# Performance work log

Measured on AMD Instinct MI355X. Metric: run time of the kernel, lower is better.

Reference implementation:

```python
import jax, jax.numpy as jnp
import numpy as np

N, L, DS, DP, H, A, Q, V = 1, 512, 384, 256, 12, 16, 4, 8
SHID = H * (DP + A + 3 * V + V)  # 3648
WC = float(np.sqrt(2.0 / (9.0 * Q)))
WL = float(np.sqrt(1.0 / 3.0))
EPS = 1e-5


def quat2rot(q):
    # q: (..., 3) partial quaternion (w fixed to 1, then normalized) -> (..., 3, 3)
    ones = jnp.ones(q.shape[:-1] + (1,), q.dtype)
    qf = jnp.concatenate([ones, q], axis=-1)
    qf = qf / jnp.linalg.norm(qf, axis=-1, keepdims=True)
    w, x, y, z = qf[..., 0], qf[..., 1], qf[..., 2], qf[..., 3]
    r0 = jnp.stack([1 - 2 * (y * y + z * z), 2 * (x * y - w * z), 2 * (x * z + w * y)], -1)
    r1 = jnp.stack([2 * (x * y + w * z), 1 - 2 * (x * x + z * z), 2 * (y * z - w * x)], -1)
    r2 = jnp.stack([2 * (x * z - w * y), 2 * (y * z + w * x), 1 - 2 * (x * x + y * y)], -1)
    return jnp.stack([r0, r1, r2], axis=-2)


def layer_norm(x, g, b):
    m = x.mean(-1, keepdims=True)
    v = ((x - m) ** 2).mean(-1, keepdims=True)
    return (x - m) / jnp.sqrt(v + EPS) * g + b


def setup_inputs() -> dict:
    key = jax.random.key(0)
    ks = jax.random.split(key, 24)
    w = lambda k, shape, s=0.02: (jax.random.normal(k, shape, jnp.float32) * s)
    return {
        'sfea': jax.random.normal(ks[0], (N, L, DS), jnp.float32),
        'pfea': jax.random.normal(ks[1], (N, L, L, DP), jnp.float32),
        'quat': jax.random.normal(ks[2], (N, L, 3), jnp.float32) * 0.1,
        'trsl': jax.random.normal(ks[3], (N, L, 3), jnp.float32),
        'Wq': w(ks[4], (DS, H * A)), 'Wk': w(ks[5], (DS, H * A)), 'Wv': w(ks[6], (DS, H * A)),
        'Wqp': w(ks[7], (DS, H * Q * 3)), 'Wkp': w(ks[8], (DS, H * Q * 3)), 'Wvp': w(ks[9], (DS, H * V * 3)),
        'Wb': w(ks[10], (DP, H)),
        'scale': jnp.ones((H,), jnp.float32),
        'Ws': w(ks[11], (SHID, DS)), 'bs': jnp.zeros((DS,), jnp.float32),
        'W1': w(ks[12], (DS, DS)), 'b1': jnp.zeros((DS,), jnp.float32),
        'W2': w(ks[13], (DS, DS)), 'b2': jnp.zeros((DS,), jnp.float32),
        'W3': w(ks[14], (DS, DS)), 'b3': jnp.zeros((DS,), jnp.float32),
        'g1': jnp.ones((DS,), jnp.float32), 'be1': jnp.zeros((DS,), jnp.float32),
        'g2': jnp.ones((DS,), jnp.float32), 'be2': jnp.zeros((DS,), jnp.float32),
    }


def reference(sfea, pfea, quat, trsl, Wq, Wk, Wv, Wqp, Wkp, Wvp, Wb, scale, Ws, bs,
              W1, b1, W2, b2, W3, b3, g1, be1, g2, be2):
    n, l = sfea.shape[0], sfea.shape[1]
    # projections
    q = (sfea @ Wq).reshape(n, l, H, A)
    k = (sfea @ Wk).reshape(n, l, H, A)
    v = (sfea @ Wv).reshape(n, l, H, A)
    qp = (sfea @ Wqp).reshape(n, l, H, Q, 3)
    kp = (sfea @ Wkp).reshape(n, l, H, Q, 3)
    vp = (sfea @ Wvp).reshape(n, l, H, V, 3)
    b = jnp.einsum('nijp,ph->nijh', pfea, Wb)
    # local frames
    rot = quat2rot(quat)  # (n, l, 3, 3)
    t = trsl[:, :, None, None, :]
    qp_g = jnp.einsum('nlij,nlhqj->nlhqi', rot, qp) + t
    kp_g = jnp.einsum('nlij,nlhqj->nlhqi', rot, kp) + t
    vp_g = jnp.einsum('nlij,nlhvj->nlhvi', rot, vp) + t
    # attention logits
    qk = jnp.einsum('nihd,njhd->nijh', q, k) / np.sqrt(A)
    diff = qp_g[:, :, None] - kp_g[:, None]  # (n, i, j, h, q, 3)
    d2 = jnp.sum(diff * diff, axis=(-1, -2))  # (n, i, j, h)
    qkp = (WC * jax.nn.softplus(scale) / 2.0) * d2
    a = jax.nn.softmax(WL * (qk + b - qkp), axis=2)  # (n, i, j, h)
    # weighted sums (einsum avoids huge broadcast intermediates)
    op = jnp.einsum('nijh,nijp->nihp', a, pfea)
    ov = jnp.einsum('nijh,njhd->nihd', a, v)
    ovp_g = jnp.einsum('nijh,njhvc->nihvc', a, vp_g)
    # map back into local frame: R^T (x - t)
    ovp = jnp.einsum('nlji,nlhvj->nlhvi', rot, ovp_g - t)
    ovp_norm = jnp.sqrt(jnp.sum(ovp * ovp, axis=-1))  # (n, l, h, v)
    shid = jnp.concatenate([op, ov, ovp.reshape(n, l, H, V * 3), ovp_norm], axis=-1)
    shid = shid.reshape(n, l, SHID)
    # output projection + residual, post-LN, MLP, post-LN (v1 path, p_drop=0)
    s = sfea + shid @ Ws + bs
    s = layer_norm(s, g1, be1)
    h = jax.nn.relu(s @ W1 + b1)
    h = jax.nn.relu(h @ W2 + b2)
    s = s + (h @ W3 + b3)
    s = layer_norm(s, g2, be2)
    return s
```

## Files before the change

kernel.cpp:

```cpp
#include <hip/hip_runtime.h>
#include <cstddef>

typedef __attribute__((ext_vector_type(8))) short short8;
typedef __attribute__((ext_vector_type(4))) float f32x4;

#define WC_CONST 0.2357022603955158f
#define WL_CONST 0.5773502691896258f

__device__ __forceinline__ unsigned short rne_bf16(float f) {
  unsigned int u = __float_as_uint(f);
  u += 0x7fffu + ((u >> 16) & 1u);
  return (unsigned short)(u >> 16);
}

__global__ __launch_bounds__(256) void concat_w_kernel(
    const float* __restrict__ Wq, const float* __restrict__ Wk, const float* __restrict__ Wv,
    const float* __restrict__ Wqp, const float* __restrict__ Wkp, const float* __restrict__ Wvp,
    float* __restrict__ Wcat) {
  int idx = blockIdx.x * 256 + threadIdx.x;
  if (idx >= 384 * 1152) return;
  int k = idx / 1152, c = idx % 1152;
  float v;
  if (c < 192)       v = Wq [k*192 + c];
  else if (c < 384)  v = Wk [k*192 + (c-192)];
  else if (c < 576)  v = Wv [k*192 + (c-384)];
  else if (c < 720)  v = Wqp[k*144 + (c-576)];
  else if (c < 864)  v = Wkp[k*144 + (c-720)];
  else               v = Wvp[k*288 + (c-864)];
  Wcat[idx] = v;
}

__global__ __launch_bounds__(256) void gemm64_kernel(
    const float* __restrict__ Amat, const float* __restrict__ Bmat, float* __restrict__ Cp,
    int M, int N, int K, int ksl) {
  __shared__ float As[16][68];
  __shared__ float Bs[16][68];
  int t = threadIdx.x;
  int bn = blockIdx.x, bm = blockIdx.y, bz = blockIdx.z;
  int k0 = bz * ksl;
  int tr = t >> 4, tc = t & 15;
  int lm = t >> 2, lk4 = (t & 3) << 2;
  int lkb = t >> 4, lnq = (t & 15) << 2;
  const float* Ab = Amat + (size_t)(bm*64 + lm) * K;
  const float* Bb = Bmat + bn*64 + lnq;
  float acc[4][4];
  #pragma unroll
  for (int a2 = 0; a2 < 4; a2++)
    #pragma unroll
    for (int b2 = 0; b2 < 4; b2++) acc[a2][b2] = 0.f;

  for (int k = k0; k < k0 + ksl; k += 16) {
    float4 av = *(const float4*)(Ab + k + lk4);
    float4 bv = *(const float4*)(Bb + (size_t)(k + lkb) * N);
    As[lk4+0][lm] = av.x; As[lk4+1][lm] = av.y; As[lk4+2][lm] = av.z; As[lk4+3][lm] = av.w;
    *(float4*)&Bs[lkb][lnq] = bv;
    __syncthreads();
    #pragma unroll
    for (int kk = 0; kk < 16; kk++) {
      float4 a4 = *(const float4*)&As[kk][tr << 2];
      float4 b4 = *(const float4*)&Bs[kk][tc << 2];
      float ar[4] = {a4.x, a4.y, a4.z, a4.w};
      float br[4] = {b4.x, b4.y, b4.z, b4.w};
      #pragma unroll
      for (int a2 = 0; a2 < 4; a2++)
        #pragma unroll
        for (int b2 = 0; b2 < 4; b2++) acc[a2][b2] += ar[a2] * br[b2];
    }
    __syncthreads();
  }
  float* Cb = Cp + (size_t)bz * M * N + (size_t)(bm*64 + (tr << 2)) * N + bn*64 + (tc << 2);
  #pragma unroll
  for (int r = 0; r < 4; r++) {
    float4 o = {acc[r][0], acc[r][1], acc[r][2], acc[r][3]};
    *(float4*)(Cb + (size_t)r * N) = o;
  }
}

__global__ __launch_bounds__(256) void reduce_kernel(
    const float* __restrict__ Cp, float* __restrict__ out, const float* __restrict__ bias,
    int relu, int MN, int N, int sk) {
  int idx = blockIdx.x * 256 + threadIdx.x;
  if (idx >= MN) return;
  float s = 0.f;
  for (int z = 0; z < sk; z++) s += Cp[(size_t)z * MN + idx];
  if (bias) s += bias[idx % N];
  if (relu) s = fmaxf(s, 0.f);
  out[idx] = s;
}

__global__ __launch_bounds__(256) void gemm32_kernel(
    const float* __restrict__ Amat, const float* __restrict__ Bmat,
    const float* __restrict__ bias,
    float* __restrict__ C, int M, int N, int K, int relu) {
  __shared__ float As[16][34];
  __shared__ float Bs[16][34];
  int t = threadIdx.x;
  int bn = blockIdx.x, bm = blockIdx.y;
  int tr = t >> 4, tc = t & 15;
  int lm = t >> 3, lk2 = (t & 7) << 1;
  int lkb = t >> 4, ln2 = (t & 15) << 1;
  const float* Ab = Amat + (size_t)(bm*32 + lm) * K;
  const float* Bb = Bmat + bn*32 + ln2;
  float a00=0.f, a01=0.f, a10=0.f, a11=0.f;
  for (int k = 0; k < K; k += 16) {
    float2 av = *(const float2*)(Ab + k + lk2);
    float2 bv = *(const float2*)(Bb + (size_t)(k + lkb) * N);
    As[lk2][lm] = av.x; As[lk2+1][lm] = av.y;
    *(float2*)&Bs[lkb][ln2] = bv;
    __syncthreads();
    #pragma unroll
    for (int kk = 0; kk < 16; kk++) {
      float2 a2 = *(const float2*)&As[kk][tr << 1];
      float2 b2 = *(const float2*)&Bs[kk][tc << 1];
      a00 += a2.x*b2.x; a01 += a2.x*b2.y; a10 += a2.y*b2.x; a11 += a2.y*b2.y;
    }
    __syncthreads();
  }
  int r0 = bm*32 + (tr << 1), c0 = bn*32 + (tc << 1);
  float bb0 = bias ? bias[c0] : 0.f, bb1 = bias ? bias[c0+1] : 0.f;
  float o00 = a00 + bb0, o01 = a01 + bb1, o10 = a10 + bb0, o11 = a11 + bb1;
  if (relu) { o00=fmaxf(o00,0.f); o01=fmaxf(o01,0.f); o10=fmaxf(o10,0.f); o11=fmaxf(o11,0.f); }
  float2 w0 = {o00, o01}, w1 = {o10, o11};
  *(float2*)(C + (size_t)r0*N + c0) = w0;
  *(float2*)(C + (size_t)(r0+1)*N + c0) = w1;
}

__global__ __launch_bounds__(64) void frames_kernel(
    const float* __restrict__ proj, const float* __restrict__ quat, const float* __restrict__ trsl,
    float* __restrict__ rotb, float* __restrict__ qpg, float* __restrict__ kpg,
    float* __restrict__ vvT) {
  int i = blockIdx.x, t = threadIdx.x;
  float q0 = quat[i*3+0], q1 = quat[i*3+1], q2 = quat[i*3+2];
  float inv = rsqrtf(1.f + q0*q0 + q1*q1 + q2*q2);
  float w = inv, x = q0*inv, y = q1*inv, z = q2*inv;
  float R00 = 1.f - 2.f*(y*y + z*z), R01 = 2.f*(x*y - w*z), R02 = 2.f*(x*z + w*y);
  float R10 = 2.f*(x*y + w*z), R11 = 1.f - 2.f*(x*x + z*z), R12 = 2.f*(y*z - w*x);
  float R20 = 2.f*(x*z - w*y), R21 = 2.f*(y*z + w*x), R22 = 1.f - 2.f*(x*x + y*y);
  float t0 = trsl[i*3+0], t1 = trsl[i*3+1], t2 = trsl[i*3+2];
  if (t == 0) {
    float* rb = rotb + i*9;
    rb[0]=R00; rb[1]=R01; rb[2]=R02; rb[3]=R10; rb[4]=R11; rb[5]=R12; rb[6]=R20; rb[7]=R21; rb[8]=R22;
  }
  for (int pt = t; pt < 96; pt += 64) {
    const float* src; float* dst;
    if (pt < 48) { src = proj + i*1152 + 576 + pt*3;      dst = qpg + i*144 + pt*3; }
    else         { src = proj + i*1152 + 720 + (pt-48)*3; dst = kpg + i*144 + (pt-48)*3; }
    float p0 = src[0], p1 = src[1], p2 = src[2];
    dst[0] = R00*p0 + R01*p1 + R02*p2 + t0;
    dst[1] = R10*p0 + R11*p1 + R12*p2 + t1;
    dst[2] = R20*p0 + R21*p1 + R22*p2 + t2;
  }
  for (int o = t; o < 480; o += 64) {
    float val;
    if (o < 192) {
      val = proj[i*1152 + 384 + o];
    } else {
      int m = o - 192;
      int vi = m / 3, c = m - vi * 3;
      const float* p = proj + i*1152 + 864 + vi*3;
      float p0 = p[0], p1 = p[1], p2 = p[2];
      val = (c == 0) ? (R00*p0 + R01*p1 + R02*p2 + t0)
          : (c == 1) ? (R10*p0 + R11*p1 + R12*p2 + t1)
                     : (R20*p0 + R21*p1 + R22*p2 + t2);
    }
    vvT[(size_t)o * 512 + i] = val;
  }
}

__global__ __launch_bounds__(256) void bgemm_kernel(
    const float* __restrict__ pfea, const float* __restrict__ Wb, float* __restrict__ bmatT) {
  __shared__ short wbf[8][64][8];
  int t = threadIdx.x;
  for (int s = t; s < 512; s += 256) {
    int ks = s >> 6, l = s & 63;
    int col = l & 15, kb = ks * 32 + ((l >> 4) << 3);
    #pragma unroll
    for (int j = 0; j < 8; j++)
      wbf[ks][l][j] = (col < 12) ? (short)rne_bf16(Wb[(kb + j) * 12 + col]) : (short)0;
  }
  __syncthreads();
  int wv = t >> 6, lane = t & 63;
  int wglob = blockIdx.x * 4 + wv;
  int row = lane & 15, kq = lane >> 4;
  for (int it = 0; it < 4; it++) {
    int tile = wglob * 4 + it;
    size_t p0 = (size_t)tile * 16;
    const float* Ab = pfea + (p0 + row) * 256 + kq * 8;
    f32x4 acc = {0.f, 0.f, 0.f, 0.f};
    #pragma unroll
    for (int ks = 0; ks < 8; ks++) {
      float4 f0 = *(const float4*)(Ab + ks * 32);
      float4 f1 = *(const float4*)(Ab + ks * 32 + 4);
      short8 af;
      af[0] = (short)rne_bf16(f0.x); af[1] = (short)rne_bf16(f0.y);
      af[2] = (short)rne_bf16(f0.z); af[3] = (short)rne_bf16(f0.w);
      af[4] = (short)rne_bf16(f1.x); af[5] = (short)rne_bf16(f1.y);
      af[6] = (short)rne_bf16(f1.z); af[7] = (short)rne_bf16(f1.w);
      short8 bfv = *(const short8*)(&wbf[ks][lane][0]);
      acc = __builtin_amdgcn_mfma_f32_16x16x32_bf16(af, bfv, acc, 0, 0, 0);
    }
    int col = lane & 15;
    if (col < 12) {
      #pragma unroll
      for (int r = 0; r < 4; r++) {
        size_t pr = p0 + kq * 4 + r;
        bmatT[(pr >> 9) * 6144 + (size_t)col * 512 + (pr & 511)] = acc[r];
      }
    }
  }
}

__device__ __forceinline__ float lt1_val(
    const float* __restrict__ proj, const float* __restrict__ kpg,
    const float* qs_, const float* qps_, float coef, int jg, int h) {
  const float4* kr = (const float4*)(proj + (size_t)jg*1152 + 192 + h*16);
  const float4* qr = (const float4*)(qs_ + h*16);
  float qk = 0.f;
  #pragma unroll
  for (int m = 0; m < 4; m++) {
    float4 kv = kr[m], qv = qr[m];
    qk += qv.x*kv.x + qv.y*kv.y + qv.z*kv.z + qv.w*kv.w;
  }
  const float4* kpr = (const float4*)(kpg + (size_t)jg*144 + h*12);
  const float4* qpr = (const float4*)(qps_ + h*12);
  float d2 = 0.f;
  #pragma unroll
  for (int m = 0; m < 3; m++) {
    float4 kv = kpr[m], qv = qpr[m];
    float dx = qv.x-kv.x, dy = qv.y-kv.y, dz = qv.z-kv.z, dw = qv.w-kv.w;
    d2 += dx*dx + dy*dy + dz*dz + dw*dw;
  }
  return qk*0.25f - coef*d2;
}

__global__ __launch_bounds__(768) void attn7_kernel(
    const float* __restrict__ proj, const float* __restrict__ qpg,
    const float* __restrict__ kpg, const float* __restrict__ pfea,
    const float* __restrict__ bmatT, const float* __restrict__ scale,
    float* __restrict__ shid, float* __restrict__ wmatT, float* __restrict__ shinv_g) {
  __shared__ float Lws[512][12];
  __shared__ __align__(16) float4 opred[12][64];
  __shared__ __align__(16) float qs[12][16];
  __shared__ __align__(16) float qps[12][12];
  __shared__ float coefs[12], sh_inv[12];

  int i = blockIdx.x, t = threadIdx.x;
  int w = t >> 6, lane = t & 63;

  for (int idx = t; idx < 192; idx += 768) qs[idx >> 4][idx & 15] = proj[i*1152 + idx];
  for (int idx = t; idx < 144; idx += 768) qps[idx / 12][idx % 12] = qpg[i*144 + idx];
  if (t < 12) coefs[t] = WC_CONST * 0.5f * log1pf(__expf(scale[t]));
  __syncthreads();

  float wvals[8];
  {
    const float* bT = bmatT + (size_t)i * 6144 + (size_t)w * 512;
    float* wT = wmatT + (size_t)i * 6144 + (size_t)w * 512;
    float cf = coefs[w];
    #pragma unroll
    for (int r = 0; r < 8; r++) {
      int j = lane + 64 * r;
      float lb = lt1_val(proj, kpg, &qs[0][0], &qps[0][0], cf, j, w);
      float val = __expf(WL_CONST * (lb + bT[j]));
      Lws[j][w] = val;
      wT[j] = val;
      wvals[r] = val;
    }
  }
  {
    float sacc = 0.f;
    #pragma unroll
    for (int r = 0; r < 8; r++) sacc += wvals[r];
    #pragma unroll
    for (int off = 32; off >= 1; off >>= 1) sacc += __shfl_xor(sacc, off);
    if (lane == 0) { sh_inv[w] = 1.0f / sacc; shinv_g[i*12 + w] = 1.0f / sacc; }
  }
  __syncthreads();

  int wp = w >> 1, half = w & 1;
  int nr = (wp < 2) ? 86 : 85;
  int off0 = half ? 4 : 0, off1 = half ? 8 : 4;
  const float* pf = pfea + (size_t)i * 131072 + (lane << 2);

  float4 opacc[6];
  #pragma unroll
  for (int c = 0; c < 6; c++) { opacc[c].x=0.f; opacc[c].y=0.f; opacc[c].z=0.f; opacc[c].w=0.f; }

  float4 pvA = *(const float4*)(pf + (size_t)wp * 256);
  float4 pvB = *(const float4*)(pf + (size_t)(wp + 6) * 256);
  float4 pvC = *(const float4*)(pf + (size_t)(wp + 12) * 256);
  float4 lwA0 = *(const float4*)&Lws[wp][off0];
  float4 lwA1 = *(const float4*)&Lws[wp][off1];

  for (int r = 0; r < nr; r++) {
    float4 pv = pvA;
    pvA = pvB; pvB = pvC;
    int jn = wp + 6 * (r + 3); if (jn > 511) jn = 511;
    pvC = *(const float4*)(pf + (size_t)jn * 256);

    float4 lw0 = lwA0, lw1 = lwA1;
    int jl = wp + 6 * (r + 1); if (jl > 511) jl = wp;
    lwA0 = *(const float4*)&Lws[jl][off0];
    lwA1 = *(const float4*)&Lws[jl][off1];

    float wv0, wv1, wv2, wv3, wv4, wv5;
    if (half == 0) { wv0=lw0.x; wv1=lw0.y; wv2=lw0.z; wv3=lw0.w; wv4=lw1.x; wv5=lw1.y; }
    else           { wv0=lw0.z; wv1=lw0.w; wv2=lw1.x; wv3=lw1.y; wv4=lw1.z; wv5=lw1.w; }

    opacc[0].x += wv0*pv.x; opacc[0].y += wv0*pv.y; opacc[0].z += wv0*pv.z; opacc[0].w += wv0*pv.w;
    opacc[1].x += wv1*pv.x; opacc[1].y += wv1*pv.y; opacc[1].z += wv1*pv.z; opacc[1].w += wv1*pv.w;
    opacc[2].x += wv2*pv.x; opacc[2].y += wv2*pv.y; opacc[2].z += wv2*pv.z; opacc[2].w += wv2*pv.w;
    opacc[3].x += wv3*pv.x; opacc[3].y += wv3*pv.y; opacc[3].z += wv3*pv.z; opacc[3].w += wv3*pv.w;
    opacc[4].x += wv4*pv.x; opacc[4].y += wv4*pv.y; opacc[4].z += wv4*pv.z; opacc[4].w += wv4*pv.w;
    opacc[5].x += wv5*pv.x; opacc[5].y += wv5*pv.y; opacc[5].z += wv5*pv.z; opacc[5].w += wv5*pv.w;
  }
  __syncthreads();

  #pragma unroll
  for (int g = 0; g < 6; g++) {
    opred[half * 6 + wp][lane] = opacc[g];
    __syncthreads();
    if (t < 128) {
      int hh = t >> 6, ll = t & 63;
      float4 s = {0.f, 0.f, 0.f, 0.f};
      #pragma unroll
      for (int w2 = 0; w2 < 6; w2++) {
        float4 v = opred[hh * 6 + w2][ll];
        s.x += v.x; s.y += v.y; s.z += v.z; s.w += v.w;
      }
      int h = g + 6 * hh;
      float isv = sh_inv[h];
      float4 o = {s.x*isv, s.y*isv, s.z*isv, s.w*isv};
      *(float4*)(shid + (size_t)i * 3648 + h * 304 + (ll << 2)) = o;
    }
    __syncthreads();
  }
}

__global__ __launch_bounds__(512) void ovph_kernel(
    const float* __restrict__ wmatT, const float* __restrict__ vvT,
    const float* __restrict__ shinv_g, const float* __restrict__ rotb,
    const float* __restrict__ trsl, float* __restrict__ shid) {
  __shared__ float ovpg_l[12][24];
  __shared__ float sh_inv[12], rot_s[9];
  int i = blockIdx.x, t = threadIdx.x;
  int w = t >> 6, lane = t & 63;
  if (t < 12) sh_inv[t] = shinv_g[i*12 + t];
  if (t >= 16 && t < 25) rot_s[t - 16] = rotb[i*9 + (t - 16)];
  __syncthreads();

  const float* wbase = wmatT + (size_t)i * 6144;
  for (int o = w * 60; o < w * 60 + 60; o++) {
    int h = (o < 192) ? (o >> 4) : ((o - 192) / 24);
    const float* wrow = wbase + (size_t)h * 512 + lane;
    const float* vrow = vvT + (size_t)o * 512 + lane;
    float acc = 0.f;
    #pragma unroll
    for (int k = 0; k < 8; k++) acc += wrow[64*k] * vrow[64*k];
    #pragma unroll
    for (int off = 32; off >= 1; off >>= 1) acc += __shfl_xor(acc, off);
    if (lane == 0) {
      float val = acc * sh_inv[h];
      if (o < 192) shid[(size_t)i * 3648 + h * 304 + 256 + (o & 15)] = val;
      else         ovpg_l[h][(o - 192) - h * 24] = val;
    }
  }
  __syncthreads();

  if (t < 96) {
    int h = t >> 3, vv = t & 7;
    float x = ovpg_l[h][vv*3+0] - trsl[i*3+0];
    float y = ovpg_l[h][vv*3+1] - trsl[i*3+1];
    float z = ovpg_l[h][vv*3+2] - trsl[i*3+2];
    float o0 = rot_s[0]*x + rot_s[3]*y + rot_s[6]*z;
    float o1 = rot_s[1]*x + rot_s[4]*y + rot_s[7]*z;
    float o2 = rot_s[2]*x + rot_s[5]*y + rot_s[8]*z;
    float* so = shid + (size_t)i*3648 + h*304 + 272 + vv*3;
    so[0] = o0; so[1] = o1; so[2] = o2;
    shid[(size_t)i*3648 + h*304 + 296 + vv] = sqrtf(o0*o0 + o1*o1 + o2*o2);
  }
}

__global__ __launch_bounds__(384) void ln384_kernel(
    const float* __restrict__ resid, const float* __restrict__ C, const float* __restrict__ bias,
    const float* __restrict__ g, const float* __restrict__ be, float* __restrict__ out) {
  int i = blockIdx.x, t = threadIdx.x;
  __shared__ float red[6];
  float x = resid[(size_t)i*384 + t] + C[(size_t)i*384 + t] + bias[t];
  float s = x;
  #pragma unroll
  for (int off = 32; off >= 1; off >>= 1) s += __shfl_xor(s, off);
  if ((t & 63) == 0) red[t >> 6] = s;
  __syncthreads();
  float m = (red[0]+red[1]+red[2]+red[3]+red[4]+red[5]) * (1.f/384.f);
  __syncthreads();
  float d = x - m;
  float v = d * d;
  #pragma unroll
  for (int off = 32; off >= 1; off >>= 1) v += __shfl_xor(v, off);
  if ((t & 63) == 0) red[t >> 6] = v;
  __syncthreads();
  float var = (red[0]+red[1]+red[2]+red[3]+red[4]+red[5]) * (1.f/384.f);
  out[(size_t)i*384 + t] = d * rsqrtf(var + 1e-5f) * g[t] + be[t];
}

extern "C" void kernel_launch(void* const* d_in, const int* in_sizes, int n_in,
                              void* d_out, int out_size, void* d_ws, size_t ws_size,
                              hipStream_t stream) {
  const float* sfea = (const float*)d_in[0];
  const float* pfea = (const float*)d_in[1];
  const float* quat = (const float*)d_in[2];
  const float* trsl = (const float*)d_in[3];
  const float* Wq   = (const float*)d_in[4];
  const float* Wk   = (const float*)d_in[5];
  const float* Wv   = (const float*)d_in[6];
  const float* Wqp  = (const float*)d_in[7];
  const float* Wkp  = (const float*)d_in[8];
  const float* Wvp  = (const float*)d_in[9];
  const float* Wb   = (const float*)d_in[10];
  const float* scale= (const float*)d_in[11];
  const float* Wsm  = (const float*)d_in[12];
  const float* bs   = (const float*)d_in[13];
  const float* W1   = (const float*)d_in[14];
  const float* b1   = (const float*)d_in[15];
  const float* W2   = (const float*)d_in[16];
  const float* b2   = (const float*)d_in[17];
  const float* W3   = (const float*)d_in[18];
  const float* b3   = (const float*)d_in[19];
  const float* g1   = (const float*)d_in[20];
  const float* be1  = (const float*)d_in[21];
  const float* g2   = (const float*)d_in[22];
  const float* be2  = (const float*)d_in[23];
  float* out = (float*)d_out;
  float* wsf = (float*)d_ws;

  float* Wcat  = wsf;
  float* proj  = Wcat + 442368;
  float* rotb  = proj + 589824;
  float* qpg   = rotb + 4608;
  float* kpg   = qpg + 73728;
  float* vvT   = kpg + 73728;
  float* big   = vvT + 245760;
  float* wmatT = big + 3145728;
  float* shinv = wmatT + 3145728;
  float* shid  = shinv + 6144;
  float* C1    = shid + 1867776;
  float* s1    = C1 + 196608;
  float* h1    = s1 + 196608;
  float* h2    = h1 + 196608;
  float* C3    = h2 + 196608;
  float* bmatT = big;
  float* cpart = big;

  concat_w_kernel<<<1728, 256, 0, stream>>>(Wq, Wk, Wv, Wqp, Wkp, Wvp, Wcat);
  gemm64_kernel<<<dim3(18, 8, 1), 256, 0, stream>>>(sfea, Wcat, proj, 512, 1152, 384, 384);
  frames_kernel<<<512, 64, 0, stream>>>(proj, quat, trsl, rotb, qpg, kpg, vvT);
  bgemm_kernel<<<1024, 256, 0, stream>>>(pfea, Wb, bmatT);
  attn7_kernel<<<512, 768, 0, stream>>>(proj, qpg, kpg, pfea, bmatT, scale, shid, wmatT, shinv);
  ovph_kernel<<<512, 512, 0, stream>>>(wmatT, vvT, shinv, rotb, trsl, shid);

  gemm64_kernel<<<dim3(6, 8, 6), 256, 0, stream>>>(shid, Wsm, cpart, 512, 384, 3648, 608);
  reduce_kernel<<<768, 256, 0, stream>>>(cpart, C1, nullptr, 0, 196608, 384, 6);
  ln384_kernel<<<512, 384, 0, stream>>>(sfea, C1, bs, g1, be1, s1);

  gemm32_kernel<<<dim3(12, 16), 256, 0, stream>>>(s1, W1, b1, h1, 512, 384, 384, 1);
  gemm32_kernel<<<dim3(12, 16), 256, 0, stream>>>(h1, W2, b2, h2, 512, 384, 384, 1);
  gemm32_kernel<<<dim3(12, 16), 256, 0, stream>>>(h2, W3, nullptr, C3, 512, 384, 384, 0);
  ln384_kernel<<<512, 384, 0, stream>>>(s1, C3, b3, g2, be2, out);
}
```

Before: 358.7 us.

## Restructure attention pfea reduction: 4 waves each own all 12 heads over j-slices

The attention kernel shrinks from 768 to 256 threads per block. Each wave now accumulates all 12 heads over a contiguous 128-row slice of j, instead of 6 heads over a strided slice. Each pfea element is therefore loaded once per block instead of twice, and the cross-wave reduction uses 4 partials instead of 6. The pfea loads use explicit double-buffered batches of 8 float4, and the softmax sums are recomputed from shared memory. In exchange the kernel uses many more registers per thread (48 accumulators plus 64 buffered floats), and it relies on two blocks per CU for latency hiding.

Result: no change. 364.6 us (+1.7%).

```diff
diff --git a/kernel.cpp b/kernel.cpp
--- a/kernel.cpp
+++ b/kernel.cpp
@@ -233,13 +233,13 @@
   return qk*0.25f - coef*d2;
 }
 
-__global__ __launch_bounds__(768) void attn7_kernel(
+__global__ __launch_bounds__(256, 2) void attn8_kernel(
     const float* __restrict__ proj, const float* __restrict__ qpg,
     const float* __restrict__ kpg, const float* __restrict__ pfea,
     const float* __restrict__ bmatT, const float* __restrict__ scale,
     float* __restrict__ shid, float* __restrict__ wmatT, float* __restrict__ shinv_g) {
   __shared__ float Lws[512][12];
-  __shared__ __align__(16) float4 opred[12][64];
+  __shared__ __align__(16) float4 opred[4][2][64];
   __shared__ __align__(16) float qs[12][16];
   __shared__ __align__(16) float qps[12][12];
   __shared__ float coefs[12], sh_inv[12];
@@ -247,88 +247,97 @@
   int i = blockIdx.x, t = threadIdx.x;
   int w = t >> 6, lane = t & 63;
 
-  for (int idx = t; idx < 192; idx += 768) qs[idx >> 4][idx & 15] = proj[i*1152 + idx];
-  for (int idx = t; idx < 144; idx += 768) qps[idx / 12][idx % 12] = qpg[i*144 + idx];
+  for (int idx = t; idx < 192; idx += 256) qs[idx >> 4][idx & 15] = proj[i*1152 + idx];
+  for (int idx = t; idx < 144; idx += 256) qps[idx / 12][idx % 12] = qpg[i*144 + idx];
   if (t < 12) coefs[t] = WC_CONST * 0.5f * log1pf(__expf(scale[t]));
   __syncthreads();
 
-  float wvals[8];
   {
-    const float* bT = bmatT + (size_t)i * 6144 + (size_t)w * 512;
-    float* wT = wmatT + (size_t)i * 6144 + (size_t)w * 512;
-    float cf = coefs[w];
-    #pragma unroll
-    for (int r = 0; r < 8; r++) {
-      int j = lane + 64 * r;
-      float lb = lt1_val(proj, kpg, &qs[0][0], &qps[0][0], cf, j, w);
-      float val = __expf(WL_CONST * (lb + bT[j]));
-      Lws[j][w] = val;
-      wT[j] = val;
-      wvals[r] = val;
-    }
-  }
-  {
-    float sacc = 0.f;
-    #pragma unroll
-    for (int r = 0; r < 8; r++) sacc += wvals[r];
-    #pragma unroll
-    for (int off = 32; off >= 1; off >>= 1) sacc += __shfl_xor(sacc, off);
-    if (lane == 0) { sh_inv[w] = 1.0f / sacc; shinv_g[i*12 + w] = 1.0f / sacc; }
-  }
-  __syncthreads();
-
-  int wp = w >> 1, half = w & 1;
-  int nr = (wp < 2) ? 86 : 85;
-  int off0 = half ? 4 : 0, off1 = half ? 8 : 4;
-  const float* pf = pfea + (size_t)i * 131072 + (lane << 2);
-
-  float4 opacc[6];
-  #pragma unroll
-  for (int c = 0; c < 6; c++) { opacc[c].x=0.f; opacc[c].y=0.f; opacc[c].z=0.f; opacc[c].w=0.f; }
-
-  float4 pvA = *(const float4*)(pf + (size_t)wp * 256);
-  float4 pvB = *(const float4*)(pf + (size_t)(wp + 6) * 256);
-  float4 pvC = *(const float4*)(pf + (size_t)(wp + 12) * 256);
-  float4 lwA0 = *(const float4*)&Lws[wp][off0];
-  float4 lwA1 = *(const float4*)&Lws[wp][off1];
-
-  for (int r = 0; r < nr; r++) {
-    float4 pv = pvA;
-    pvA = pvB; pvB = pvC;
-    int jn = wp + 6 * (r + 3); if (jn > 511) jn = 511;
-    pvC = *(const float4*)(pf + (size_t)jn * 256);
-
-    float4 lw0 = lwA0, lw1 = lwA1;
-    int jl = wp + 6 * (r + 1); if (jl > 511) jl = wp;
-    lwA0 = *(const float4*)&Lws[jl][off0];
-    lwA1 = *(const float4*)&Lws[jl][off1];
-
-    float wv0, wv1, wv2, wv3, wv4, wv5;
-    if (half == 0) { wv0=lw0.x; wv1=lw0.y; wv2=lw0.z; wv3=lw0.w; wv4=lw1.x; wv5=lw1.y; }
-    else           { wv0=lw0.z; wv1=lw0.w; wv2=lw1.x; wv3=lw1.y; wv4=lw1.z; wv5=lw1.w; }
-
-    opacc[0].x += wv0*pv.x; opacc[0].y += wv0*pv.y; opacc[0].z += wv0*pv.z; opacc[0].w += wv0*pv.w;
-    opacc[1].x += wv1*pv.x; opacc[1].y += wv1*pv.y; opacc[1].z += wv1*pv.z; opacc[1].w += wv1*pv.w;
-    opacc[2].x += wv2*pv.x; opacc[2].y += wv2*pv.y; opacc[2].z += wv2*pv.z; opacc[2].w += wv2*pv.w;
-    opacc[3].x += wv3*pv.x; opacc[3].y += wv3*pv.y; opacc[3].z += wv3*pv.z; opacc[3].w += wv3*pv.w;
-    opacc[4].x += wv4*pv.x; opacc[4].y += wv4*pv.y; opacc[4].z += wv4*pv.z; opacc[4].w += wv4*pv.w;
-    opacc[5].x += wv5*pv.x; opacc[5].y += wv5*pv.y; opacc[5].z += wv5*pv.z; opacc[5].w += wv5*pv.w;
-  }
+    const float* bT = bmatT + (size_t)i * 6144;
+    float* wT = wmatT + (size_t)i * 6144;
+    for (int r = 0; r < 24; r++) {
+      int o = t + r * 256;
+      int j = o & 511, h = o >> 9;
+      float lb = lt1_val(proj, kpg, &qs[0][0], &qps[0][0], coefs[h], j, h);
+      float val = __expf(WL_CONST * (lb + bT[o]));
+      Lws[j][h] = val;
+      wT[o] = val;
+    }
+  }
+  __syncthreads();
+
+  for (int h = w; h < 12; h += 4) {
+    float s = 0.f;
+    #pragma unroll
+    for (int r = 0; r < 8; r++) s += Lws[lane + (r << 6)][h];
+    #pragma unroll
+    for (int off = 32; off >= 1; off >>= 1) s += __shfl_xor(s, off);
+    if (lane == 0) { sh_inv[h] = 1.0f / s; shinv_g[i*12 + h] = 1.0f / s; }
+  }
+  __syncthreads();
+
+  float4 opacc[12];
+  #pragma unroll
+  for (int h = 0; h < 12; h++) { opacc[h].x=0.f; opacc[h].y=0.f; opacc[h].z=0.f; opacc[h].w=0.f; }
+
+  int j0 = w * 128;
+  const float* pf = pfea + (size_t)i * 131072 + (size_t)j0 * 256 + (lane << 2);
+
+  float4 bufA[8], bufB[8];
+  #pragma unroll
+  for (int r = 0; r < 8; r++) bufA[r] = *(const float4*)(pf + (size_t)r * 256);
+
+  #define COMPUTE_BATCH(BUF, JB)                                                  \
+    _Pragma("unroll")                                                             \
+    for (int r = 0; r < 8; r++) {                                                 \
+      const float4* lwp = (const float4*)&Lws[(JB) + r][0];                       \
+      float4 lw0 = lwp[0], lw1 = lwp[1], lw2 = lwp[2];                            \
+      float4 pv = BUF[r];                                                         \
+      opacc[0].x += lw0.x*pv.x; opacc[0].y += lw0.x*pv.y; opacc[0].z += lw0.x*pv.z; opacc[0].w += lw0.x*pv.w; \
+      opacc[1].x += lw0.y*pv.x; opacc[1].y += lw0.y*pv.y; opacc[1].z += lw0.y*pv.z; opacc[1].w += lw0.y*pv.w; \
+      opacc[2].x += lw0.z*pv.x; opacc[2].y += lw0.z*pv.y; opacc[2].z += lw0.z*pv.z; opacc[2].w += lw0.z*pv.w; \
+      opacc[3].x += lw0.w*pv.x; opacc[3].y += lw0.w*pv.y; opacc[3].z += lw0.w*pv.z; opacc[3].w += lw0.w*pv.w; \
+      opacc[4].x += lw1.x*pv.x; opacc[4].y += lw1.x*pv.y; opacc[4].z += lw1.x*pv.z; opacc[4].w += lw1.x*pv.w; \
+      opacc[5].x += lw1.y*pv.x; opacc[5].y += lw1.y*pv.y; opacc[5].z += lw1.y*pv.z; opacc[5].w += lw1.y*pv.w; \
+      opacc[6].x += lw1.z*pv.x; opacc[6].y += lw1.z*pv.y; opacc[6].z += lw1.z*pv.z; opacc[6].w += lw1.z*pv.w; \
+      opacc[7].x += lw1.w*pv.x; opacc[7].y += lw1.w*pv.y; opacc[7].z += lw1.w*pv.z; opacc[7].w += lw1.w*pv.w; \
+      opacc[8].x += lw2.x*pv.x; opacc[8].y += lw2.x*pv.y; opacc[8].z += lw2.x*pv.z; opacc[8].w += lw2.x*pv.w; \
+      opacc[9].x += lw2.y*pv.x; opacc[9].y += lw2.y*pv.y; opacc[9].z += lw2.y*pv.z; opacc[9].w += lw2.y*pv.w; \
+      opacc[10].x += lw2.z*pv.x; opacc[10].y += lw2.z*pv.y; opacc[10].z += lw2.z*pv.z; opacc[10].w += lw2.z*pv.w; \
+      opacc[11].x += lw2.w*pv.x; opacc[11].y += lw2.w*pv.y; opacc[11].z += lw2.w*pv.z; opacc[11].w += lw2.w*pv.w; \
+    }
+
+  for (int bp = 0; bp < 8; bp++) {
+    {
+      const float* baseB = pf + (size_t)(bp * 16 + 8) * 256;
+      #pragma unroll
+      for (int r = 0; r < 8; r++) bufB[r] = *(const float4*)(baseB + (size_t)r * 256);
+    }
+    COMPUTE_BATCH(bufA, j0 + bp * 16)
+    if (bp < 7) {
+      const float* baseA = pf + (size_t)(bp * 16 + 16) * 256;
+      #pragma unroll
+      for (int r = 0; r < 8; r++) bufA[r] = *(const float4*)(baseA + (size_t)r * 256);
+    }
+    COMPUTE_BATCH(bufB, j0 + bp * 16 + 8)
+  }
+  #undef COMPUTE_BATCH
   __syncthreads();
 
   #pragma unroll
   for (int g = 0; g < 6; g++) {
-    opred[half * 6 + wp][lane] = opacc[g];
+    opred[w][0][lane] = opacc[2*g + 0];
+    opred[w][1][lane] = opacc[2*g + 1];
     __syncthreads();
     if (t < 128) {
       int hh = t >> 6, ll = t & 63;
       float4 s = {0.f, 0.f, 0.f, 0.f};
       #pragma unroll
-      for (int w2 = 0; w2 < 6; w2++) {
-        float4 v = opred[hh * 6 + w2][ll];
+      for (int w2 = 0; w2 < 4; w2++) {
+        float4 v = opred[w2][hh][ll];
         s.x += v.x; s.y += v.y; s.z += v.z; s.w += v.w;
       }
-      int h = g + 6 * hh;
+      int h = 2*g + hh;
       float isv = sh_inv[h];
       float4 o = {s.x*isv, s.y*isv, s.z*isv, s.w*isv};
       *(float4*)(shid + (size_t)i * 3648 + h * 304 + (ll << 2)) = o;
@@ -456,7 +465,7 @@
   gemm64_kernel<<<dim3(18, 8, 1), 256, 0, stream>>>(sfea, Wcat, proj, 512, 1152, 384, 384);
   frames_kernel<<<512, 64, 0, stream>>>(proj, quat, trsl, rotb, qpg, kpg, vvT);
   bgemm_kernel<<<1024, 256, 0, stream>>>(pfea, Wb, bmatT);
-  attn7_kernel<<<512, 768, 0, stream>>>(proj, qpg, kpg, pfea, bmatT, scale, shid, wmatT, shinv);
+  attn8_kernel<<<512, 256, 0, stream>>>(proj, qpg, kpg, pfea, bmatT, scale, shid, wmatT, shinv);
   ovph_kernel<<<512, 512, 0, stream>>>(wmatT, vvT, shinv, rotb, trsl, shid);
 
   gemm64_kernel<<<dim3(6, 8, 6), 256, 0, stream>>>(shid, Wsm, cpart, 512, 384, 3648, 608);
```
